# Performance work log

Measured on AMD Instinct MI355X. Metric: run time of the kernel, lower is better.

The kernel has to match this reference:

```python
import jax, jax.numpy as jnp
import numpy as np

B, L, H, E, V, T = 64, 512, 512, 512, 64, 200  # L must equal H (attention broadcast in source)
SOS_TOKEN = 0


def setup_inputs() -> dict:
    key = jax.random.key(0)
    ks = jax.random.split(key, 16)
    s = 0.05
    return {
        "seq_embeddings": jax.random.normal(ks[0], (B, L, H), jnp.float32),
        "key_w": jax.random.normal(ks[1], (H, H), jnp.float32) * s,
        "key_b": jax.random.normal(ks[2], (H,), jnp.float32) * s,
        "value_w": jax.random.normal(ks[3], (H, H), jnp.float32) * s,
        "value_b": jax.random.normal(ks[4], (H,), jnp.float32) * s,
        "char_emb": jax.random.normal(ks[5], (V, E), jnp.float32) * s,
        "w_ih": jax.random.normal(ks[6], (4 * H, E + H), jnp.float32) * s,
        "w_hh": jax.random.normal(ks[7], (4 * H, H), jnp.float32) * s,
        "b_ih": jax.random.normal(ks[8], (4 * H,), jnp.float32) * s,
        "b_hh": jax.random.normal(ks[9], (4 * H,), jnp.float32) * s,
        "cdn_w": jax.random.normal(ks[10], (V, 2 * H), jnp.float32) * s,
        "cdn_b": jax.random.normal(ks[11], (V,), jnp.float32) * s,
        "seq_embedding_lengths": jax.random.randint(ks[12], (B,), 1, L + 1),
        "batch_y": jax.random.randint(ks[13], (B, T), 0, V),
    }


def reference(seq_embeddings, key_w, key_b, value_w, value_b, char_emb,
              w_ih, w_hh, b_ih, b_hh, cdn_w, cdn_b,
              seq_embedding_lengths, batch_y):
    b, l, h = seq_embeddings.shape
    t = batch_y.shape[1]
    v = cdn_w.shape[0]
    dt = seq_embeddings.dtype

    # Attention: since logits = sum_l (keys*q) and context = sum_l (values*w),
    # both factor through the masked sum over L -> precompute once (loop-invariant).
    mask = (jnp.arange(l)[None, :] < seq_embedding_lengths[:, None]).astype(dt)  # (B, L)
    msum = jnp.einsum('blh,bl->bh', seq_embeddings, mask)                        # (B, H)
    keysum = msum @ key_w.T + l * key_b                                          # sum of keys over L
    valsum = msum @ value_w.T + l * value_b                                      # sum of values over L
    scale = jnp.sqrt(jnp.asarray(h, dt))

    def attend(q):  # q: (B, H); softmax over the key_dim axis, as in source
        w = jax.nn.softmax(keysum * q / scale, axis=1)
        return valsum * w

    ctx0 = attend(jnp.zeros((b, h), dt))
    h0 = jnp.zeros((b, h), dt)
    c0 = jnp.zeros((b, h), dt)

    # prev token at step i: SOS at i=1, batch_y[:, i-1] afterwards (tf_rate=1.0)
    prev_ys = jnp.concatenate(
        [jnp.full((1, b), SOS_TOKEN, dtype=batch_y.dtype), batch_y[:, 1:t - 1].T], axis=0)  # (T-1, B)

    def step(carry, y_prev):
        hh, cc, ctx = carry
        x = jnp.concatenate([char_emb[y_prev], ctx], axis=1)           # (B, E+H)
        gates = x @ w_ih.T + b_ih + hh @ w_hh.T + b_hh                 # (B, 4H)
        i_g, f_g, g_g, o_g = jnp.split(gates, 4, axis=1)
        cc = jax.nn.sigmoid(f_g) * cc + jax.nn.sigmoid(i_g) * jnp.tanh(g_g)
        hh = jax.nn.sigmoid(o_g) * jnp.tanh(cc)
        ctx = attend(hh)
        logit = jnp.concatenate([hh, ctx], axis=1) @ cdn_w.T + cdn_b   # (B, V)
        return (hh, cc, ctx), logit

    _, logits_seq = jax.lax.scan(step, (h0, c0, ctx0), prev_ys)        # (T-1, B, V)
    logits = jnp.concatenate(
        [jnp.zeros((1, b, v), dt), logits_seq], axis=0).transpose(1, 0, 2)  # (B, T, V)

    # multinomial sampling of output symbols (random in source; seeded here)
    samp = jax.random.categorical(jax.random.key(1), logits[:, 1:, :], axis=-1)
    symbols = jnp.concatenate(
        [jnp.zeros((b, 1), samp.dtype), samp], axis=1)                 # (B, T)
    return logits, symbols
```

## Files before the change

kernel.cpp:

```cpp
#include <hip/hip_runtime.h>
#include <math.h>

#define NB 64
#define NH 512
#define NV 64
#define NT 200
#define NSTEP 199
#define GBLK 256
#define GTHR 512

#define RLX   __ATOMIC_RELAXED
#define AGENT __HIP_MEMORY_SCOPE_AGENT

typedef float f4v __attribute__((ext_vector_type(4)));

__device__ inline float gumbel_tf(unsigned f){
  const unsigned ksc[3] = {0u, 1u, 0x1BD11BDBu};
  unsigned x0 = 0u + ksc[0];
  unsigned x1 = f  + ksc[1];
  const int R0[4] = {13,15,26,6};
  const int R1[4] = {17,29,16,24};
  #pragma unroll
  for (int i = 0; i < 5; ++i){
    #pragma unroll
    for (int r = 0; r < 4; ++r){
      int rot = (i & 1) ? R1[r] : R0[r];
      x0 += x1;
      x1 = (x1 << rot) | (x1 >> (32 - rot));
      x1 ^= x0;
    }
    x0 += ksc[(i+1)%3];
    x1 += ksc[(i+2)%3] + (unsigned)(i+1);
  }
  unsigned bits = x0 ^ x1;
  float u = __uint_as_float((bits >> 9) | 0x3F800000u) - 1.0f;
  u = fmaxf(u, 1.17549435e-38f);
  return -logf(-logf(u));
}

__device__ inline float sigf(float x){ return 1.0f/(1.0f + expf(-x)); }

__device__ inline void gbar2(unsigned* flags, unsigned* gen, int blk, unsigned tgt){
  asm volatile("s_waitcnt vmcnt(0)" ::: "memory");
  __syncthreads();
  const int tid = threadIdx.x;
  if (tid == 0){
    unsigned o = __hip_atomic_exchange(&flags[blk*16], tgt, RLX, AGENT);
    asm volatile("" :: "v"(o));
  }
  if (blk == 128){
    if (tid < 256){
      while (__hip_atomic_load(&flags[tid*16], RLX, AGENT) < tgt){
        __builtin_amdgcn_s_sleep(1);
      }
    }
    __syncthreads();
    if (tid == 0){
      unsigned o = __hip_atomic_exchange(gen, tgt, RLX, AGENT);
      asm volatile("" :: "v"(o));
    }
  }
  if (tid == 0){
    while (__hip_atomic_load(gen, RLX, AGENT) < tgt){
      __builtin_amdgcn_s_sleep(1);
    }
  }
  __syncthreads();
}

__device__ inline float blk_red_max(float v, float* scr){
  #pragma unroll
  for (int m = 1; m < 64; m <<= 1) v = fmaxf(v, __shfl_xor(v, m, 64));
  if ((threadIdx.x & 63) == 0) scr[threadIdx.x >> 6] = v;
  __syncthreads();
  float r = scr[0];
  #pragma unroll
  for (int i = 1; i < 8; ++i) r = fmaxf(r, scr[i]);
  __syncthreads();
  return r;
}
__device__ inline float blk_red_sum(float v, float* scr){
  #pragma unroll
  for (int m = 1; m < 64; m <<= 1) v += __shfl_xor(v, m, 64);
  if ((threadIdx.x & 63) == 0) scr[threadIdx.x >> 6] = v;
  __syncthreads();
  float r = 0.f;
  #pragma unroll
  for (int i = 0; i < 8; ++i) r += scr[i];
  __syncthreads();
  return r;
}

__global__ void k_msum_part(const float* __restrict__ emb, const int* __restrict__ lens,
                            float* __restrict__ part){
  int blk = blockIdx.x, b = blk >> 3, lc = blk & 7;
  int len = lens[b];
  int l0 = lc*64, l1 = len < l0+64 ? len : l0+64;
  for (int h = threadIdx.x; h < 512; h += 256){
    float a = 0.f;
    for (int l = l0; l < l1; ++l) a += emb[(b*512 + l)*512 + h];
    part[blk*512 + h] = a;
  }
}
__global__ void k_msum(const float* __restrict__ part, float* __restrict__ msumT){
  int b = blockIdx.x;
  for (int h = threadIdx.x; h < 512; h += 256){
    float a = 0.f;
    #pragma unroll
    for (int lc = 0; lc < 8; ++lc) a += part[(b*8+lc)*512 + h];
    msumT[h*64 + b] = a;
  }
}
__global__ void k_kv(const float* __restrict__ msumT,
                     const float* __restrict__ kw, const float* __restrict__ kb,
                     const float* __restrict__ vw, const float* __restrict__ vb,
                     float* __restrict__ keysum, float* __restrict__ valsum){
  int which = blockIdx.x >> 7;
  int i = ((blockIdx.x & 127) << 2) + (threadIdx.x >> 6);
  int b = threadIdx.x & 63;
  const float* W = which ? vw : kw;
  float a = 0.f;
  for (int h = 0; h < 512; ++h) a = fmaf(msumT[h*64+b], W[i*512+h], a);
  float bias = which ? vb[i] : kb[i];
  float* out = which ? valsum : keysum;
  out[b*512 + i] = a + 512.0f*bias;
}
__global__ void k_ceT(const float* __restrict__ ce, float* __restrict__ ceT){
  int idx = blockIdx.x*256 + threadIdx.x;
  if (idx < 32768){ int v = idx >> 9, e = idx & 511; ceT[e*64 + v] = ce[v*512 + e]; }
}
__global__ void k_tok(const float* __restrict__ ceT, const float* __restrict__ w_ih,
                      const float* __restrict__ b_ih, const float* __restrict__ b_hh,
                      float* __restrict__ tok){
  int idx = blockIdx.x*256 + threadIdx.x;
  int v = idx & 63, row = idx >> 6;
  float a = 0.f;
  for (int e = 0; e < 512; ++e) a = fmaf(ceT[e*64+v], w_ih[row*1024 + e], a);
  tok[v*2048 + row] = a + b_ih[row] + b_hh[row];
}
__global__ void k_init(const float* __restrict__ valsum, const float* __restrict__ cdn_w,
                       float* __restrict__ cdnT, float* __restrict__ xT,
                       float* __restrict__ out, unsigned* __restrict__ bar){
  int idx = blockIdx.x*256 + threadIdx.x;
  if (idx < 65536){
    int v = idx >> 10, k = idx & 1023;
    cdnT[k*64 + v] = cdn_w[idx];
  } else if (idx < 98304){
    int r = idx - 65536; int j = r >> 6, b = r & 63;
    xT[j*64 + b] = valsum[b*512 + j] * (1.0f/512.0f);
  } else if (idx < 131072){
    xT[idx - 65536] = 0.f;
  } else if (idx < 135168){
    int r = idx - 131072; int b = r >> 6, v = r & 63;
    out[b*12800 + v] = 0.f;
  } else if (idx < 135232){
    int b = idx - 135168;
    out[819200 + b*200] = 0.f;
  } else if (idx < 139392){
    bar[idx - 135232] = 0u;
  }
}

__global__ __launch_bounds__(GTHR, 2) void k_loop(
    const float* __restrict__ w_ih, const float* __restrict__ w_hh,
    const int* __restrict__ batch_y, const float* __restrict__ tok,
    const float* __restrict__ keysum, const float* __restrict__ valsum,
    const float* __restrict__ cdnT, const float* __restrict__ cdn_b,
    float* __restrict__ xT, float* __restrict__ out,
    unsigned* __restrict__ bar){
  __shared__ float W_lds[1024][8];
  __shared__ float red[8][8][64];
  __shared__ float gates_lds[8][64];
  __shared__ float cc_lds[2][64];
  __shared__ float pb_h[512], pb_c[512];
  __shared__ float pb_lp[8][64];
  __shared__ float scr[8];

  unsigned* flags = bar;
  unsigned* gen   = bar + 4096;

  const int tid = threadIdx.x;
  const int blk = blockIdx.x;

  for (int idx = tid; idx < 8192; idx += GTHR){
    int k = idx >> 3, r = idx & 7;
    int g = r >> 1, c = r & 1;
    int row = g*512 + blk*2 + c;
    W_lds[k][r] = (k < 512) ? w_ih[row*1024 + 512 + k] : w_hh[row*512 + (k - 512)];
  }
  if (tid < 128) cc_lds[tid >> 6][tid & 63] = 0.0f;
  __syncthreads();

  const int w = tid >> 6, l = tid & 63, kg = l >> 4, bg = l & 15;
  const float SCALE = 22.627416997969522f;
  int p = 0;

#define ISS1(R, JJ) do{ const float* _p = xin + (((kbase + (JJ)*4) << 6) | (bg << 2)); \
  asm volatile("global_load_dwordx4 %0, %1, off sc0 sc1" : "=v"(R) : "v"(_p)); }while(0)
#define ISS8(P, J0) do{ ISS1(P##0,(J0)+0);ISS1(P##1,(J0)+1);ISS1(P##2,(J0)+2);ISS1(P##3,(J0)+3); \
  ISS1(P##4,(J0)+4);ISS1(P##5,(J0)+5);ISS1(P##6,(J0)+6);ISS1(P##7,(J0)+7); }while(0)
#define CMP1(R, JJ) do{ int _k = kbase + (JJ)*4; \
  f4v _wA = *(const f4v*)&W_lds[_k][0]; f4v _wB = *(const f4v*)&W_lds[_k][4]; \
  float _wv[8] = {_wA.x,_wA.y,_wA.z,_wA.w,_wB.x,_wB.y,_wB.z,_wB.w}; \
  float _xv[4] = {R.x,R.y,R.z,R.w}; \
  _Pragma("unroll") for (int _r = 0; _r < 8; ++_r){ \
    _Pragma("unroll") for (int _q = 0; _q < 4; ++_q) \
      acc[_r][_q] = fmaf(_wv[_r], _xv[_q], acc[_r][_q]); } }while(0)
#define CMP8(P, J0) do{ CMP1(P##0,(J0)+0);CMP1(P##1,(J0)+1);CMP1(P##2,(J0)+2);CMP1(P##3,(J0)+3); \
  CMP1(P##4,(J0)+4);CMP1(P##5,(J0)+5);CMP1(P##6,(J0)+6);CMP1(P##7,(J0)+7); }while(0)
#define WAITV(N) do{ asm volatile("s_waitcnt vmcnt(" #N ")" ::: "memory"); \
  __builtin_amdgcn_sched_barrier(0); }while(0)

  for (int s = 0; s < NSTEP; ++s){
    const float* xin  = xT + p*65536;
    float*       xout = xT + (p^1)*65536;

    const int rr = tid >> 6, rb = tid & 63;
    int yprev = (s == 0) ? 0 : batch_y[rb*200 + s];
    float tokval = tok[yprev*2048 + (rr >> 1)*512 + blk*2 + (rr & 1)];

    float acc[8][4];
    #pragma unroll
    for (int r = 0; r < 8; ++r)
      #pragma unroll
      for (int q = 0; q < 4; ++q) acc[r][q] = 0.f;

    const int kbase = w*128 + kg;
    {
      f4v A0,A1,A2,A3,A4,A5,A6,A7,B0,B1,B2,B3,B4,B5,B6,B7;
      ISS8(A, 0);
      ISS8(B, 8);
      WAITV(8); CMP8(A, 0);
      ISS8(A, 16);
      WAITV(8); CMP8(B, 8);
      ISS8(B, 24);
      WAITV(8); CMP8(A, 16);
      WAITV(0); CMP8(B, 24);
    }

    #pragma unroll
    for (int r = 0; r < 8; ++r)
      #pragma unroll
      for (int q = 0; q < 4; ++q){
        float v = acc[r][q];
        v += __shfl_xor(v, 16, 64);
        v += __shfl_xor(v, 32, 64);
        acc[r][q] = v;
      }
    if (l < 16){
      #pragma unroll
      for (int r = 0; r < 8; ++r)
        *(float4*)&red[w][r][bg*4] = make_float4(acc[r][0], acc[r][1], acc[r][2], acc[r][3]);
    }
    __syncthreads();
    {
      float g = 0.f;
      #pragma unroll
      for (int ww = 0; ww < 8; ++ww) g += red[ww][rr][rb];
      gates_lds[rr][rb] = g + tokval;
    }
    __syncthreads();
    if (tid < 128){
      int c = tid >> 6, b = tid & 63;
      float ig = gates_lds[0 + c][b];
      float fg = gates_lds[2 + c][b];
      float gg = gates_lds[4 + c][b];
      float og = gates_lds[6 + c][b];
      float cprev = cc_lds[c][b];
      float cnew = sigf(fg)*cprev + sigf(ig)*tanhf(gg);
      float hnew = sigf(og)*tanhf(cnew);
      cc_lds[c][b] = cnew;
      float oldh = __hip_atomic_exchange(&xout[(512 + blk*2 + c)*64 + b], hnew, RLX, AGENT);
      asm volatile("" :: "v"(oldh));
    }
    gbar2(flags, gen, blk, (unsigned)(2*s + 1));

    if (blk < 64){
      int b = blk;
      int jj = tid;
      float h = __hip_atomic_load(&xout[(512 + jj)*64 + b], RLX, AGENT);
      pb_h[jj] = h;
      float sc = (keysum[b*512 + jj] * h) / SCALE;
      float m = blk_red_max(sc, scr);
      float e = expf(sc - m);
      float S = blk_red_sum(e, scr);
      float cx = valsum[b*512 + jj] * (e / S);
      pb_c[jj] = cx;
      float oldc = __hip_atomic_exchange(&xout[jj*64 + b], cx, RLX, AGENT);
      asm volatile("" :: "v"(oldc));
      __syncthreads();
      int kq = tid >> 6, v = tid & 63;
      float part = 0.f;
      for (int k = kq*128; k < kq*128 + 128; ++k){
        float xh = (k < 512) ? pb_h[k] : pb_c[k - 512];
        part = fmaf(cdnT[k*64 + v], xh, part);
      }
      pb_lp[kq][v] = part;
      __syncthreads();
      if (tid < 64){
        int v2 = tid;
        float logit = cdn_b[v2];
        #pragma unroll
        for (int q = 0; q < 8; ++q) logit += pb_lp[q][v2];
        out[b*12800 + (s+1)*64 + v2] = logit;
        float z = gumbel_tf((unsigned)((b*199 + s)*64 + v2)) + logit;
        int idx = v2;
        #pragma unroll
        for (int mm = 1; mm < 64; mm <<= 1){
          float oz = __shfl_xor(z, mm, 64);
          int   oi = __shfl_xor(idx, mm, 64);
          if (oz > z || (oz == z && oi < idx)){ z = oz; idx = oi; }
        }
        if (v2 == 0) out[819200 + b*200 + (s+1)] = (float)idx;
      }
    }
    gbar2(flags, gen, blk, (unsigned)(2*s + 2));
    p ^= 1;
  }
#undef ISS1
#undef ISS8
#undef CMP1
#undef CMP8
#undef WAITV
}

extern "C" void kernel_launch(void* const* d_in, const int* in_sizes, int n_in,
                              void* d_out, int out_size, void* d_ws, size_t ws_size,
                              hipStream_t stream){
  const float* seq     = (const float*)d_in[0];
  const float* key_w   = (const float*)d_in[1];
  const float* key_b   = (const float*)d_in[2];
  const float* value_w = (const float*)d_in[3];
  const float* value_b = (const float*)d_in[4];
  const float* char_e  = (const float*)d_in[5];
  const float* w_ih    = (const float*)d_in[6];
  const float* w_hh    = (const float*)d_in[7];
  const float* b_ih    = (const float*)d_in[8];
  const float* b_hh    = (const float*)d_in[9];
  const float* cdn_w   = (const float*)d_in[10];
  const float* cdn_b   = (const float*)d_in[11];
  const int*   lens    = (const int*)d_in[12];
  const int*   batch_y = (const int*)d_in[13];
  float* out = (float*)d_out;
  float* ws  = (float*)d_ws;

  float* msum_part = ws;
  float* msumT     = ws + 262144;
  float* keysum    = ws + 294912;
  float* valsum    = ws + 327680;
  float* tok       = ws + 360448;
  float* cdnT      = ws + 491520;
  float* ceT       = ws + 557056;
  float* xT        = ws + 589824;
  unsigned* bar    = (unsigned*)(ws + 720896);

  k_msum_part<<<512, 256, 0, stream>>>(seq, lens, msum_part);
  k_msum     <<<64,  256, 0, stream>>>(msum_part, msumT);
  k_kv       <<<256, 256, 0, stream>>>(msumT, key_w, key_b, value_w, value_b, keysum, valsum);
  k_ceT      <<<128, 256, 0, stream>>>(char_e, ceT);
  k_tok      <<<512, 256, 0, stream>>>(ceT, w_ih, b_ih, b_hh, tok);
  k_init     <<<545, 256, 0, stream>>>(valsum, cdn_w, cdnT, xT, out, bar);

  k_loop<<<GBLK, GTHR, 0, stream>>>(w_ih, w_hh, batch_y, tok, keysum, valsum,
                                    cdnT, cdn_b, xT, out, bar);
  (void)in_sizes; (void)n_in; (void)out_size; (void)ws_size;
}
```

Before: 5.927 ms.

## Use per-step ring buffer for recurrent state to allow cached loads

```diff
diff --git a/kernel.cpp b/kernel.cpp
--- a/kernel.cpp
+++ b/kernel.cpp
@@ -161,12 +161,13 @@
   }
 }
 
+template<bool RING>
 __global__ __launch_bounds__(GTHR, 2) void k_loop(
     const float* __restrict__ w_ih, const float* __restrict__ w_hh,
     const int* __restrict__ batch_y, const float* __restrict__ tok,
     const float* __restrict__ keysum, const float* __restrict__ valsum,
     const float* __restrict__ cdnT, const float* __restrict__ cdn_b,
-    float* __restrict__ xT, float* __restrict__ out,
+    float* __restrict__ xbase, float* __restrict__ out,
     unsigned* __restrict__ bar){
   __shared__ float W_lds[1024][8];
   __shared__ float red[8][8][64];
@@ -176,6 +177,10 @@
   __shared__ float pb_lp[8][64];
   __shared__ float scr[8];
 
+  if (RING){
+    __builtin_amdgcn_fence(__ATOMIC_ACQUIRE, "agent");
+  }
+
   unsigned* flags = bar;
   unsigned* gen   = bar + 4096;
 
@@ -196,7 +201,8 @@
   int p = 0;
 
 #define ISS1(R, JJ) do{ const float* _p = xin + (((kbase + (JJ)*4) << 6) | (bg << 2)); \
-  asm volatile("global_load_dwordx4 %0, %1, off sc0 sc1" : "=v"(R) : "v"(_p)); }while(0)
+  if (RING) asm volatile("global_load_dwordx4 %0, %1, off"         : "=v"(R) : "v"(_p)); \
+  else      asm volatile("global_load_dwordx4 %0, %1, off sc0 sc1" : "=v"(R) : "v"(_p)); }while(0)
 #define ISS8(P, J0) do{ ISS1(P##0,(J0)+0);ISS1(P##1,(J0)+1);ISS1(P##2,(J0)+2);ISS1(P##3,(J0)+3); \
   ISS1(P##4,(J0)+4);ISS1(P##5,(J0)+5);ISS1(P##6,(J0)+6);ISS1(P##7,(J0)+7); }while(0)
 #define CMP1(R, JJ) do{ int _k = kbase + (JJ)*4; \
@@ -212,8 +218,15 @@
   __builtin_amdgcn_sched_barrier(0); }while(0)
 
   for (int s = 0; s < NSTEP; ++s){
-    const float* xin  = xT + p*65536;
-    float*       xout = xT + (p^1)*65536;
+    const float* xin;
+    float*       xout;
+    if (RING){
+      xin  = xbase + (size_t)s*65536;
+      xout = xbase + (size_t)(s + 1)*65536;
+    } else {
+      xin  = xbase + p*65536;
+      xout = xbase + (p^1)*65536;
+    }
 
     const int rr = tid >> 6, rb = tid & 63;
     int yprev = (s == 0) ? 0 : batch_y[rb*200 + s];
@@ -353,15 +366,25 @@
   float* ceT       = ws + 557056;
   float* xT        = ws + 589824;
   unsigned* bar    = (unsigned*)(ws + 720896);
+  float* xring     = ws + 725056;
+
+  const size_t need = (size_t)(725056 + 201*65536) * sizeof(float);
+  const bool ring = (ws_size >= need);
+  float* xbase = ring ? xring : xT;
 
   k_msum_part<<<512, 256, 0, stream>>>(seq, lens, msum_part);
   k_msum     <<<64,  256, 0, stream>>>(msum_part, msumT);
   k_kv       <<<256, 256, 0, stream>>>(msumT, key_w, key_b, value_w, value_b, keysum, valsum);
   k_ceT      <<<128, 256, 0, stream>>>(char_e, ceT);
   k_tok      <<<512, 256, 0, stream>>>(ceT, w_ih, b_ih, b_hh, tok);
-  k_init     <<<545, 256, 0, stream>>>(valsum, cdn_w, cdnT, xT, out, bar);
-
-  k_loop<<<GBLK, GTHR, 0, stream>>>(w_ih, w_hh, batch_y, tok, keysum, valsum,
-                                    cdnT, cdn_b, xT, out, bar);
+  k_init     <<<545, 256, 0, stream>>>(valsum, cdn_w, cdnT, xbase, out, bar);
+
+  if (ring){
+    k_loop<true><<<GBLK, GTHR, 0, stream>>>(w_ih, w_hh, batch_y, tok, keysum, valsum,
+                                            cdnT, cdn_b, xbase, out, bar);
+  } else {
+    k_loop<false><<<GBLK, GTHR, 0, stream>>>(w_ih, w_hh, batch_y, tok, keysum, valsum,
+                                             cdnT, cdn_b, xbase, out, bar);
+  }
   (void)in_sizes; (void)n_in; (void)out_size; (void)ws_size;
 }
```

New measurement: 5.953 ms. No clear change (+0.4%).

## Halve persistent grid and replace centralized grid barrier with per-block flag polling

Applied to the files above, without the earlier changes.

```diff
diff --git a/kernel.cpp b/kernel.cpp
--- a/kernel.cpp
+++ b/kernel.cpp
@@ -6,7 +6,7 @@
 #define NV 64
 #define NT 200
 #define NSTEP 199
-#define GBLK 256
+#define GBLK 128
 #define GTHR 512
 
 #define RLX   __ATOMIC_RELAXED
@@ -40,28 +40,9 @@
 
 __device__ inline float sigf(float x){ return 1.0f/(1.0f + expf(-x)); }
 
-__device__ inline void gbar2(unsigned* flags, unsigned* gen, int blk, unsigned tgt){
-  asm volatile("s_waitcnt vmcnt(0)" ::: "memory");
-  __syncthreads();
-  const int tid = threadIdx.x;
-  if (tid == 0){
-    unsigned o = __hip_atomic_exchange(&flags[blk*16], tgt, RLX, AGENT);
-    asm volatile("" :: "v"(o));
-  }
-  if (blk == 128){
-    if (tid < 256){
-      while (__hip_atomic_load(&flags[tid*16], RLX, AGENT) < tgt){
-        __builtin_amdgcn_s_sleep(1);
-      }
-    }
-    __syncthreads();
-    if (tid == 0){
-      unsigned o = __hip_atomic_exchange(gen, tgt, RLX, AGENT);
-      asm volatile("" :: "v"(o));
-    }
-  }
-  if (tid == 0){
-    while (__hip_atomic_load(gen, RLX, AGENT) < tgt){
+__device__ inline void gbar_wait(unsigned* flags, unsigned tgt){
+  if (threadIdx.x < GBLK){
+    while (__hip_atomic_load(&flags[threadIdx.x*16], RLX, AGENT) < tgt){
       __builtin_amdgcn_s_sleep(1);
     }
   }
@@ -161,34 +142,38 @@
   }
 }
 
+struct Smem {
+  float W[1024][16];
+  float red[8][16][64];
+  float gates[16][64];
+  float cc[4][64];
+  float pb_h[512];
+  float pb_c[512];
+  float pb_lp[8][64];
+  float scr[8];
+};
+
 __global__ __launch_bounds__(GTHR, 2) void k_loop(
     const float* __restrict__ w_ih, const float* __restrict__ w_hh,
     const int* __restrict__ batch_y, const float* __restrict__ tok,
     const float* __restrict__ keysum, const float* __restrict__ valsum,
     const float* __restrict__ cdnT, const float* __restrict__ cdn_b,
     float* __restrict__ xT, float* __restrict__ out,
-    unsigned* __restrict__ bar){
-  __shared__ float W_lds[1024][8];
-  __shared__ float red[8][8][64];
-  __shared__ float gates_lds[8][64];
-  __shared__ float cc_lds[2][64];
-  __shared__ float pb_h[512], pb_c[512];
-  __shared__ float pb_lp[8][64];
-  __shared__ float scr[8];
-
-  unsigned* flags = bar;
-  unsigned* gen   = bar + 4096;
+    unsigned* __restrict__ flags){
+  extern __shared__ char smem_raw[];
+  Smem& S = *reinterpret_cast<Smem*>(smem_raw);
 
   const int tid = threadIdx.x;
   const int blk = blockIdx.x;
-
-  for (int idx = tid; idx < 8192; idx += GTHR){
-    int k = idx >> 3, r = idx & 7;
-    int g = r >> 1, c = r & 1;
-    int row = g*512 + blk*2 + c;
-    W_lds[k][r] = (k < 512) ? w_ih[row*1024 + 512 + k] : w_hh[row*512 + (k - 512)];
-  }
-  if (tid < 128) cc_lds[tid >> 6][tid & 63] = 0.0f;
+  const bool HASB = (blk < 64);
+
+  for (int idx = tid; idx < 16384; idx += GTHR){
+    int k = idx >> 4, r = idx & 15;
+    int g = r >> 2, c = r & 3;
+    int row = g*512 + blk*4 + c;
+    S.W[k][r] = (k < 512) ? w_ih[row*1024 + 512 + k] : w_hh[row*512 + (k - 512)];
+  }
+  if (tid < 256) S.cc[tid >> 6][tid & 63] = 0.0f;
   __syncthreads();
 
   const int w = tid >> 6, l = tid & 63, kg = l >> 4, bg = l & 15;
@@ -200,10 +185,12 @@
 #define ISS8(P, J0) do{ ISS1(P##0,(J0)+0);ISS1(P##1,(J0)+1);ISS1(P##2,(J0)+2);ISS1(P##3,(J0)+3); \
   ISS1(P##4,(J0)+4);ISS1(P##5,(J0)+5);ISS1(P##6,(J0)+6);ISS1(P##7,(J0)+7); }while(0)
 #define CMP1(R, JJ) do{ int _k = kbase + (JJ)*4; \
-  f4v _wA = *(const f4v*)&W_lds[_k][0]; f4v _wB = *(const f4v*)&W_lds[_k][4]; \
-  float _wv[8] = {_wA.x,_wA.y,_wA.z,_wA.w,_wB.x,_wB.y,_wB.z,_wB.w}; \
+  f4v _wA = *(const f4v*)&S.W[_k][0];  f4v _wB = *(const f4v*)&S.W[_k][4]; \
+  f4v _wC = *(const f4v*)&S.W[_k][8];  f4v _wD = *(const f4v*)&S.W[_k][12]; \
+  float _wv[16] = {_wA.x,_wA.y,_wA.z,_wA.w,_wB.x,_wB.y,_wB.z,_wB.w, \
+                   _wC.x,_wC.y,_wC.z,_wC.w,_wD.x,_wD.y,_wD.z,_wD.w}; \
   float _xv[4] = {R.x,R.y,R.z,R.w}; \
-  _Pragma("unroll") for (int _r = 0; _r < 8; ++_r){ \
+  _Pragma("unroll") for (int _r = 0; _r < 16; ++_r){ \
     _Pragma("unroll") for (int _q = 0; _q < 4; ++_q) \
       acc[_r][_q] = fmaf(_wv[_r], _xv[_q], acc[_r][_q]); } }while(0)
 #define CMP8(P, J0) do{ CMP1(P##0,(J0)+0);CMP1(P##1,(J0)+1);CMP1(P##2,(J0)+2);CMP1(P##3,(J0)+3); \
@@ -214,14 +201,16 @@
   for (int s = 0; s < NSTEP; ++s){
     const float* xin  = xT + p*65536;
     float*       xout = xT + (p^1)*65536;
+    const unsigned t1 = (unsigned)(2*s + 1), t2 = (unsigned)(2*s + 2);
 
     const int rr = tid >> 6, rb = tid & 63;
     int yprev = (s == 0) ? 0 : batch_y[rb*200 + s];
-    float tokval = tok[yprev*2048 + (rr >> 1)*512 + blk*2 + (rr & 1)];
-
-    float acc[8][4];
+    float tok1 = tok[yprev*2048 + (rr >> 2)*512 + blk*4 + (rr & 3)];
+    float tok2 = tok[yprev*2048 + ((rr + 8) >> 2)*512 + blk*4 + ((rr + 8) & 3)];
+
+    float acc[16][4];
     #pragma unroll
-    for (int r = 0; r < 8; ++r)
+    for (int r = 0; r < 16; ++r)
       #pragma unroll
       for (int q = 0; q < 4; ++q) acc[r][q] = 0.f;
 
@@ -239,7 +228,7 @@
     }
 
     #pragma unroll
-    for (int r = 0; r < 8; ++r)
+    for (int r = 0; r < 16; ++r)
       #pragma unroll
       for (int q = 0; q < 4; ++q){
         float v = acc[r][q];
@@ -249,59 +238,71 @@
       }
     if (l < 16){
       #pragma unroll
-      for (int r = 0; r < 8; ++r)
-        *(float4*)&red[w][r][bg*4] = make_float4(acc[r][0], acc[r][1], acc[r][2], acc[r][3]);
+      for (int r = 0; r < 16; ++r)
+        *(float4*)&S.red[w][r][bg*4] = make_float4(acc[r][0], acc[r][1], acc[r][2], acc[r][3]);
     }
     __syncthreads();
     {
-      float g = 0.f;
+      float g1 = 0.f, g2 = 0.f;
       #pragma unroll
-      for (int ww = 0; ww < 8; ++ww) g += red[ww][rr][rb];
-      gates_lds[rr][rb] = g + tokval;
+      for (int ww = 0; ww < 8; ++ww){
+        g1 += S.red[ww][rr][rb];
+        g2 += S.red[ww][rr + 8][rb];
+      }
+      S.gates[rr][rb]     = g1 + tok1;
+      S.gates[rr + 8][rb] = g2 + tok2;
     }
     __syncthreads();
-    if (tid < 128){
+    if (tid < 256){
       int c = tid >> 6, b = tid & 63;
-      float ig = gates_lds[0 + c][b];
-      float fg = gates_lds[2 + c][b];
-      float gg = gates_lds[4 + c][b];
-      float og = gates_lds[6 + c][b];
-      float cprev = cc_lds[c][b];
+      float ig = S.gates[0  + c][b];
+      float fg = S.gates[4  + c][b];
+      float gg = S.gates[8  + c][b];
+      float og = S.gates[12 + c][b];
+      float cprev = S.cc[c][b];
       float cnew = sigf(fg)*cprev + sigf(ig)*tanhf(gg);
       float hnew = sigf(og)*tanhf(cnew);
-      cc_lds[c][b] = cnew;
-      float oldh = __hip_atomic_exchange(&xout[(512 + blk*2 + c)*64 + b], hnew, RLX, AGENT);
+      S.cc[c][b] = cnew;
+      float oldh = __hip_atomic_exchange(&xout[(512 + blk*4 + c)*64 + b], hnew, RLX, AGENT);
       asm volatile("" :: "v"(oldh));
     }
-    gbar2(flags, gen, blk, (unsigned)(2*s + 1));
-
-    if (blk < 64){
+
+    asm volatile("s_waitcnt vmcnt(0)" ::: "memory");
+    __syncthreads();
+    if (tid == 0){
+      unsigned o = __hip_atomic_exchange(&flags[blk*16], HASB ? t1 : t2, RLX, AGENT);
+      asm volatile("" :: "v"(o));
+    }
+
+    if (HASB){
+      gbar_wait(flags, t1);
+
       int b = blk;
       int jj = tid;
       float h = __hip_atomic_load(&xout[(512 + jj)*64 + b], RLX, AGENT);
-      pb_h[jj] = h;
+      S.pb_h[jj] = h;
       float sc = (keysum[b*512 + jj] * h) / SCALE;
-      float m = blk_red_max(sc, scr);
+      float m = blk_red_max(sc, S.scr);
       float e = expf(sc - m);
-      float S = blk_red_sum(e, scr);
-      float cx = valsum[b*512 + jj] * (e / S);
-      pb_c[jj] = cx;
+      float Ssum = blk_red_sum(e, S.scr);
+      float cx = valsum[b*512 + jj] * (e / Ssum);
+      S.pb_c[jj] = cx;
       float oldc = __hip_atomic_exchange(&xout[jj*64 + b], cx, RLX, AGENT);
       asm volatile("" :: "v"(oldc));
       __syncthreads();
       int kq = tid >> 6, v = tid & 63;
       float part = 0.f;
       for (int k = kq*128; k < kq*128 + 128; ++k){
-        float xh = (k < 512) ? pb_h[k] : pb_c[k - 512];
+        float xh = (k < 512) ? S.pb_h[k] : S.pb_c[k - 512];
         part = fmaf(cdnT[k*64 + v], xh, part);
       }
-      pb_lp[kq][v] = part;
+      S.pb_lp[kq][v] = part;
       __syncthreads();
       if (tid < 64){
         int v2 = tid;
         float logit = cdn_b[v2];
         #pragma unroll
-        for (int q = 0; q < 8; ++q) logit += pb_lp[q][v2];
+        for (int q = 0; q < 8; ++q) logit += S.pb_lp[q][v2];
         out[b*12800 + (s+1)*64 + v2] = logit;
         float z = gumbel_tf((unsigned)((b*199 + s)*64 + v2)) + logit;
         int idx = v2;
@@ -313,8 +314,16 @@
         }
         if (v2 == 0) out[819200 + b*200 + (s+1)] = (float)idx;
       }
-    }
-    gbar2(flags, gen, blk, (unsigned)(2*s + 2));
+
+      asm volatile("s_waitcnt vmcnt(0)" ::: "memory");
+      __syncthreads();
+      if (tid == 0){
+        unsigned o = __hip_atomic_exchange(&flags[blk*16], t2, RLX, AGENT);
+        asm volatile("" :: "v"(o));
+      }
+    }
+
+    gbar_wait(flags, t2);
     p ^= 1;
   }
 #undef ISS1
@@ -354,6 +363,14 @@
   float* xT        = ws + 589824;
   unsigned* bar    = (unsigned*)(ws + 720896);
 
+  static int lds_attr_set = 0;
+  if (!lds_attr_set){
+    hipFuncSetAttribute((const void*)k_loop,
+                        hipFuncAttributeMaxDynamicSharedMemorySize,
+                        (int)sizeof(Smem));
+    lds_attr_set = 1;
+  }
+
   k_msum_part<<<512, 256, 0, stream>>>(seq, lens, msum_part);
   k_msum     <<<64,  256, 0, stream>>>(msum_part, msumT);
   k_kv       <<<256, 256, 0, stream>>>(msumT, key_w, key_b, value_w, value_b, keysum, valsum);
@@ -361,7 +378,7 @@
   k_tok      <<<512, 256, 0, stream>>>(ceT, w_ih, b_ih, b_hh, tok);
   k_init     <<<545, 256, 0, stream>>>(valsum, cdn_w, cdnT, xT, out, bar);
 
-  k_loop<<<GBLK, GTHR, 0, stream>>>(w_ih, w_hh, batch_y, tok, keysum, valsum,
-                                    cdnT, cdn_b, xT, out, bar);
+  k_loop<<<GBLK, GTHR, sizeof(Smem), stream>>>(w_ih, w_hh, batch_y, tok, keysum, valsum,
+                                               cdnT, cdn_b, xT, out, bar);
   (void)in_sizes; (void)n_in; (void)out_size; (void)ws_size;
 }
```

Result: slower. 9.087 ms (+53.3%).

## Replace centralized grid barriers with per-block flag polling split by data dependency

Applied to the files above, without the earlier changes.

```diff
diff --git a/kernel.cpp b/kernel.cpp
--- a/kernel.cpp
+++ b/kernel.cpp
@@ -11,6 +11,7 @@
 
 #define RLX   __ATOMIC_RELAXED
 #define AGENT __HIP_MEMORY_SCOPE_AGENT
+#define WGRP  __HIP_MEMORY_SCOPE_WORKGROUP
 
 typedef float f4v __attribute__((ext_vector_type(4)));
 
@@ -40,32 +41,14 @@
 
 __device__ inline float sigf(float x){ return 1.0f/(1.0f + expf(-x)); }
 
-__device__ inline void gbar2(unsigned* flags, unsigned* gen, int blk, unsigned tgt){
-  asm volatile("s_waitcnt vmcnt(0)" ::: "memory");
-  __syncthreads();
-  const int tid = threadIdx.x;
-  if (tid == 0){
-    unsigned o = __hip_atomic_exchange(&flags[blk*16], tgt, RLX, AGENT);
-    asm volatile("" :: "v"(o));
-  }
-  if (blk == 128){
-    if (tid < 256){
-      while (__hip_atomic_load(&flags[tid*16], RLX, AGENT) < tgt){
-        __builtin_amdgcn_s_sleep(1);
-      }
-    }
-    __syncthreads();
-    if (tid == 0){
-      unsigned o = __hip_atomic_exchange(gen, tgt, RLX, AGENT);
-      asm volatile("" :: "v"(o));
-    }
-  }
-  if (tid == 0){
-    while (__hip_atomic_load(gen, RLX, AGENT) < tgt){
+__device__ inline void poll256(unsigned* flags, unsigned tgt){
+  const int l = threadIdx.x & 63;
+  #pragma unroll
+  for (int j = 0; j < 4; ++j){
+    while (__hip_atomic_load(&flags[(l*4 + j)*16], RLX, AGENT) < tgt){
       __builtin_amdgcn_s_sleep(1);
     }
   }
-  __syncthreads();
 }
 
 __device__ inline float blk_red_max(float v, float* scr){
@@ -167,7 +150,7 @@
     const float* __restrict__ keysum, const float* __restrict__ valsum,
     const float* __restrict__ cdnT, const float* __restrict__ cdn_b,
     float* __restrict__ xT, float* __restrict__ out,
-    unsigned* __restrict__ bar){
+    unsigned* __restrict__ flags){
   __shared__ float W_lds[1024][8];
   __shared__ float red[8][8][64];
   __shared__ float gates_lds[8][64];
@@ -175,13 +158,13 @@
   __shared__ float pb_h[512], pb_c[512];
   __shared__ float pb_lp[8][64];
   __shared__ float scr[8];
-
-  unsigned* flags = bar;
-  unsigned* gen   = bar + 4096;
+  __shared__ int done_h, done_c, done_pb;
 
   const int tid = threadIdx.x;
   const int blk = blockIdx.x;
-
+  const bool HASB = (blk < 64);
+
+  if (tid == 0){ done_h = 0; done_c = 0; done_pb = 0; }
   for (int idx = tid; idx < 8192; idx += GTHR){
     int k = idx >> 3, r = idx & 7;
     int g = r >> 1, c = r & 1;
@@ -193,7 +176,6 @@
 
   const int w = tid >> 6, l = tid & 63, kg = l >> 4, bg = l & 15;
   const float SCALE = 22.627416997969522f;
-  int p = 0;
 
 #define ISS1(R, JJ) do{ const float* _p = xin + (((kbase + (JJ)*4) << 6) | (bg << 2)); \
   asm volatile("global_load_dwordx4 %0, %1, off sc0 sc1" : "=v"(R) : "v"(_p)); }while(0)
@@ -212,8 +194,31 @@
   __builtin_amdgcn_sched_barrier(0); }while(0)
 
   for (int s = 0; s < NSTEP; ++s){
-    const float* xin  = xT + p*65536;
-    float*       xout = xT + (p^1)*65536;
+    const float* xin  = xT + (size_t)(s & 1)*65536;
+    float*       xout = xT + (size_t)((s + 1) & 1)*65536;
+    const unsigned t1 = (unsigned)(2*s + 1), t2 = (unsigned)(2*s + 2);
+    const unsigned tgt_h = (s == 0) ? 0u : (unsigned)(2*s - 1);
+    const unsigned tgt_c = (s == 0) ? 0u : (unsigned)(2*s);
+
+    if (w >= 4){
+      if (w == 4){
+        poll256(flags, tgt_h);
+        __hip_atomic_store(&done_h, s + 1, RLX, WGRP);
+      } else {
+        while (__hip_atomic_load(&done_h, RLX, WGRP) < s + 1){
+          __builtin_amdgcn_s_sleep(1);
+        }
+      }
+    } else {
+      if (w == 0){
+        poll256(flags, tgt_c);
+        __hip_atomic_store(&done_c, s + 1, RLX, WGRP);
+      } else {
+        while (__hip_atomic_load(&done_c, RLX, WGRP) < s + 1){
+          __builtin_amdgcn_s_sleep(1);
+        }
+      }
+    }
 
     const int rr = tid >> 6, rb = tid & 63;
     int yprev = (s == 0) ? 0 : batch_y[rb*200 + s];
@@ -273,9 +278,24 @@
       float oldh = __hip_atomic_exchange(&xout[(512 + blk*2 + c)*64 + b], hnew, RLX, AGENT);
       asm volatile("" :: "v"(oldh));
     }
-    gbar2(flags, gen, blk, (unsigned)(2*s + 1));
-
-    if (blk < 64){
+
+    asm volatile("s_waitcnt vmcnt(0)" ::: "memory");
+    __syncthreads();
+    if (tid == 0){
+      unsigned o = __hip_atomic_exchange(&flags[blk*16], HASB ? t1 : t2, RLX, AGENT);
+      asm volatile("" :: "v"(o));
+    }
+
+    if (HASB){
+      if (w == 4){
+        poll256(flags, t1);
+        __hip_atomic_store(&done_pb, s + 1, RLX, WGRP);
+      } else {
+        while (__hip_atomic_load(&done_pb, RLX, WGRP) < s + 1){
+          __builtin_amdgcn_s_sleep(1);
+        }
+      }
+
       int b = blk;
       int jj = tid;
       float h = __hip_atomic_load(&xout[(512 + jj)*64 + b], RLX, AGENT);
@@ -313,9 +333,14 @@
         }
         if (v2 == 0) out[819200 + b*200 + (s+1)] = (float)idx;
       }
-    }
-    gbar2(flags, gen, blk, (unsigned)(2*s + 2));
-    p ^= 1;
+
+      asm volatile("s_waitcnt vmcnt(0)" ::: "memory");
+      __syncthreads();
+      if (tid == 0){
+        unsigned o = __hip_atomic_exchange(&flags[blk*16], t2, RLX, AGENT);
+        asm volatile("" :: "v"(o));
+      }
+    }
   }
 #undef ISS1
 #undef ISS8
```

Measured after the change: 5.922 ms. Within noise of the previous version (-0.1%).
